# Kernel optimization log

Hardware: AMD Instinct MI355X
Metric: run time of the kernel (lower is better)

Reference implementation:

```python
import jax, jax.numpy as jnp
import numpy as np

B, L, D, V, K, H, HD, FFN = 64, 512, 256, 32000, 6, 4, 64, 512

def _ln(x, g, b):
    mu = x.mean(-1, keepdims=True)
    v = ((x - mu) ** 2).mean(-1, keepdims=True)
    return (x - mu) / jnp.sqrt(v + 1e-5) * g + b

def _pool(x, mask):
    # attention pooling: last real token attends over full sequence
    lengths = mask.sum(1)
    last = jnp.maximum(lengths - 1, 0)
    q = x[jnp.arange(x.shape[0]), last]                      # [B,D]
    scores = jnp.einsum('bd,bld->bl', q, x)
    scores = jnp.where(mask, scores, -60000.0)
    a = jax.nn.softmax(scores, axis=-1)
    return jnp.einsum('bl,bld->bd', a, x)

def _expert(x, mask, ln1g, ln1b, Wqkv, bqkv, Wo, bo, ln2g, ln2b, W1, b1, W2, b2):
    # pre-LN transformer block, eval mode (dropout = identity)
    Bx, Lx, _ = x.shape
    h = _ln(x, ln1g, ln1b)
    qkv = h @ Wqkv.T + bqkv                                   # [B,L,3D]
    q, k, v = jnp.split(qkv, 3, axis=-1)
    q = q.reshape(Bx, Lx, H, HD).transpose(0, 2, 1, 3)
    k = k.reshape(Bx, Lx, H, HD).transpose(0, 2, 1, 3)
    v = v.reshape(Bx, Lx, H, HD).transpose(0, 2, 1, 3)
    s = jnp.einsum('bhqd,bhkd->bhqk', q, k) / jnp.sqrt(jnp.float32(HD))
    s = jnp.where(mask[:, None, None, :], s, -1e9)            # key_padding_mask
    a = jax.nn.softmax(s, axis=-1)
    o = jnp.einsum('bhqk,bhkd->bhqd', a, v).transpose(0, 2, 1, 3).reshape(Bx, Lx, D)
    x = x + o @ Wo.T + bo
    h2 = _ln(x, ln2g, ln2b)
    ff = jax.nn.gelu(h2 @ W1.T + b1, approximate=False) @ W2.T + b2
    return x + ff

def _gru(z, m, Wih, Whh, bih, bhh):
    # torch.nn.GRUCell semantics
    gi = z @ Wih.T + bih
    gh = m @ Whh.T + bhh
    ir, iz, inn = jnp.split(gi, 3, axis=-1)
    hr, hz, hn = jnp.split(gh, 3, axis=-1)
    r = jax.nn.sigmoid(ir + hr)
    u = jax.nn.sigmoid(iz + hz)
    n = jnp.tanh(inn + r * hn)
    return (1.0 - u) * n + u * m

def setup_inputs():
    key = jax.random.key(0)
    ks = jax.random.split(key, 24)
    def nrm(k, shape, s=0.02):
        return jax.random.normal(k, shape, jnp.float32) * s
    lengths = jax.random.randint(ks[0], (B,), 1, L + 1)
    mask = jnp.arange(L)[None, :] < lengths[:, None]          # prefix mask, >=1 real token
    tokens = jnp.where(mask, jax.random.randint(ks[1], (B, L), 1, V), 0)
    return dict(
        tokens=tokens, mask=mask,
        tok_emb=nrm(ks[2], (V, D)).at[0].set(0.0),            # padding_idx=0
        pos_emb=nrm(ks[3], (L, D)),
        emb_ln_g=jnp.ones((D,)), emb_ln_b=jnp.zeros((D,)),
        ln1_g=jnp.ones((K, D)), ln1_b=jnp.zeros((K, D)),
        Wqkv=nrm(ks[4], (K, 3 * D, D)), bqkv=jnp.zeros((K, 3 * D)),
        Wo=nrm(ks[5], (K, D, D)), bo=jnp.zeros((K, D)),
        ln2_g=jnp.ones((K, D)), ln2_b=jnp.zeros((K, D)),
        W1=nrm(ks[6], (K, FFN, D)), b1=jnp.zeros((K, FFN)),
        W2=nrm(ks[7], (K, D, FFN)), b2=jnp.zeros((K, D)),
        gru_Wih=nrm(ks[8], (3 * D, D)), gru_Whh=nrm(ks[9], (3 * D, D)),
        gru_bih=jnp.zeros((3 * D,)), gru_bhh=jnp.zeros((3 * D,)),
        cls_W=nrm(ks[10], (V, D)), cls_b=jnp.zeros((V,)),
    )

def reference(tokens, mask, tok_emb, pos_emb, emb_ln_g, emb_ln_b, ln1_g, ln1_b, Wqkv, bqkv, Wo, bo, ln2_g, ln2_b, W1, b1, W2, b2, gru_Wih, gru_Whh, gru_bih, gru_bhh, cls_W, cls_b):
    x = _ln(tok_emb[tokens] + pos_emb[None, :tokens.shape[1]], emb_ln_g, emb_ln_b)
    m = jnp.zeros((tokens.shape[0], D), x.dtype)
    # sequential routing / phase-1: n_iter = K, chosen = t % K for all samples, no halting
    for t in range(K):
        e = t % K
        x = _expert(x, mask, ln1_g[e], ln1_b[e], Wqkv[e], bqkv[e], Wo[e], bo[e],
                    ln2_g[e], ln2_b[e], W1[e], b1[e], W2[e], b2[e])
        z = _pool(x, mask)
        m = _gru(z, m, gru_Wih, gru_Whh, gru_bih, gru_bhh)    # GRU memory update
    return _pool(x, mask) @ cls_W.T + cls_b                   # [B, V] logits
```

## Files before the change

### kernel.cpp

```cpp
#include <hip/hip_runtime.h>
#include <hip/hip_bf16.h>

#define BB 64
#define LL 512
#define DD 256
#define VV 32000
#define KK 6
#define HH 4
#define FF 512
#define MM (BB * LL)

typedef __hip_bfloat16 bf16;
typedef unsigned short ushort_t;
typedef __attribute__((ext_vector_type(8))) __bf16 bf16x8;
typedef __attribute__((ext_vector_type(4))) float f32x4;
#define MFMA __builtin_amdgcn_mfma_f32_16x16x32_bf16

__device__ __forceinline__ ushort_t f2bfbits(float x) {
  return __builtin_bit_cast(unsigned short, (__bf16)x);
}
__device__ __forceinline__ unsigned pkbf(float lo, float hi) {
  return (unsigned)f2bfbits(lo) | ((unsigned)f2bfbits(hi) << 16);
}
union U8 { unsigned u[4]; bf16x8 v; };

__device__ __forceinline__ void gl_lds16(const ushort_t* g, ushort_t* l) {
  __builtin_amdgcn_global_load_lds(
      (const __attribute__((address_space(1))) unsigned int*)g,
      (__attribute__((address_space(3))) unsigned int*)l, 16, 0, 0);
}

__device__ __forceinline__ float blk_sum(float v, float* red) {
  #pragma unroll
  for (int o = 32; o > 0; o >>= 1) v += __shfl_down(v, o, 64);
  __syncthreads();
  if ((threadIdx.x & 63) == 0) red[threadIdx.x >> 6] = v;
  __syncthreads();
  return red[0] + red[1] + red[2] + red[3];
}

__global__ __launch_bounds__(256) void k_lens(const int* __restrict__ tokens, int* __restrict__ lens) {
  __shared__ float red[4];
  int b = blockIdx.x, t = threadIdx.x;
  float c = (tokens[b * LL + t] != 0 ? 1.f : 0.f) + (tokens[b * LL + 256 + t] != 0 ? 1.f : 0.f);
  float s = blk_sum(c, red);
  if (t == 0) lens[b] = (int)(s + 0.5f);
}

__global__ __launch_bounds__(64) void k_order(const int* __restrict__ lens, int* __restrict__ order) {
  int b = threadIdx.x;
  __shared__ int L[64];
  int len = lens[b];
  L[b] = len;
  __syncthreads();
  int rank = 0;
  for (int i = 0; i < 64; i++) {
    int li = L[i];
    if (li > len || (li == len && i < b)) rank++;
  }
  order[rank] = b;
}

__global__ __launch_bounds__(256) void k_embed4(const int* __restrict__ tokens,
                                                const float* __restrict__ tok_emb,
                                                const float* __restrict__ pos_emb,
                                                const float* __restrict__ g,
                                                const float* __restrict__ be,
                                                const float* __restrict__ g1,
                                                const float* __restrict__ b1,
                                                float* __restrict__ X,
                                                bf16* __restrict__ H) {
  int wid = threadIdx.x >> 6, lane = threadIdx.x & 63;
  int row = blockIdx.x * 4 + wid;
  int l = row & (LL - 1);
  int tok = tokens[row];
  float4 a = *reinterpret_cast<const float4*>(tok_emb + (size_t)tok * DD + lane * 4);
  float4 p = *reinterpret_cast<const float4*>(pos_emb + (size_t)l * DD + lane * 4);
  float4 v = {a.x + p.x, a.y + p.y, a.z + p.z, a.w + p.w};
  float s = v.x + v.y + v.z + v.w;
  float q = v.x * v.x + v.y * v.y + v.z * v.z + v.w * v.w;
  #pragma unroll
  for (int o = 32; o > 0; o >>= 1) { s += __shfl_xor(s, o, 64); q += __shfl_xor(q, o, 64); }
  float mu = s * (1.f / DD);
  float rstd = rsqrtf(q * (1.f / DD) - mu * mu + 1e-5f);
  float4 gv = *reinterpret_cast<const float4*>(g + lane * 4);
  float4 bv = *reinterpret_cast<const float4*>(be + lane * 4);
  float4 o4 = {(v.x - mu) * rstd * gv.x + bv.x, (v.y - mu) * rstd * gv.y + bv.y,
               (v.z - mu) * rstd * gv.z + bv.z, (v.w - mu) * rstd * gv.w + bv.w};
  *reinterpret_cast<float4*>(X + (size_t)row * DD + lane * 4) = o4;
  float s2 = o4.x + o4.y + o4.z + o4.w;
  float q2 = o4.x * o4.x + o4.y * o4.y + o4.z * o4.z + o4.w * o4.w;
  #pragma unroll
  for (int o = 32; o > 0; o >>= 1) { s2 += __shfl_xor(s2, o, 64); q2 += __shfl_xor(q2, o, 64); }
  float mu2 = s2 * (1.f / DD);
  float rstd2 = rsqrtf(q2 * (1.f / DD) - mu2 * mu2 + 1e-5f);
  float4 g1v = *reinterpret_cast<const float4*>(g1 + lane * 4);
  float4 b1v = *reinterpret_cast<const float4*>(b1 + lane * 4);
  ushort4 h4;
  h4.x = f2bfbits((o4.x - mu2) * rstd2 * g1v.x + b1v.x);
  h4.y = f2bfbits((o4.y - mu2) * rstd2 * g1v.y + b1v.y);
  h4.z = f2bfbits((o4.z - mu2) * rstd2 * g1v.z + b1v.z);
  h4.w = f2bfbits((o4.w - mu2) * rstd2 * g1v.w + b1v.w);
  *reinterpret_cast<ushort4*>((ushort_t*)H + (size_t)row * DD + lane * 4) = h4;
}

__global__ __launch_bounds__(256) void k_cvtw(const float* __restrict__ w0, const float* __restrict__ w1,
                                              const float* __restrict__ w2, const float* __restrict__ w3,
                                              ushort_t* __restrict__ d) {
  int i = (blockIdx.x * 256 + threadIdx.x) * 4;
  const float* s; int off;
  if (i < 196608)      { s = w0; off = i; }
  else if (i < 262144) { s = w1; off = i - 196608; }
  else if (i < 393216) { s = w2; off = i - 262144; }
  else                 { s = w3; off = i - 393216; }
  float4 v = *reinterpret_cast<const float4*>(s + off);
  ushort4 o;
  o.x = f2bfbits(v.x); o.y = f2bfbits(v.y); o.z = f2bfbits(v.z); o.w = f2bfbits(v.w);
  *reinterpret_cast<ushort4*>(d + i) = o;
}

template <int MT, int NT, int KD, bool GELU, bool RES, bool OUTBF16, bool FUSELN>
__global__ __launch_bounds__(256) void k_mgemm(const ushort_t* __restrict__ A,
                                               const ushort_t* __restrict__ Wb,
                                               const float* __restrict__ bias,
                                               const float* __restrict__ res,
                                               void* __restrict__ outp,
                                               ushort_t* __restrict__ Hout,
                                               const float* __restrict__ lng,
                                               const float* __restrict__ lnb,
                                               const int* __restrict__ lens,
                                               int Ndim) {
  constexpr int JF = (MT == 128) ? (NT / 32) : (NT / 64);
  constexpr int AR = MT / 64, BR = NT / 64;
  constexpr int L = AR + BR;
  constexpr int NK = KD / 32;
  int n0 = blockIdx.x * NT, m0 = blockIdx.y * MT;
  if ((m0 & (LL - 1)) >= lens[m0 >> 9]) return;
  __shared__ __align__(16) ushort_t As[3][MT * 32];
  __shared__ __align__(16) ushort_t Bs[3][NT * 32];
  int t = threadIdx.x, lane = t & 63, w = t >> 6;
  int wr = (MT == 128) ? (w >> 1) * 64 : 0;
  int wc = (MT == 128) ? (w & 1) * (NT / 2) : w * (NT / 4);
  int fr = lane & 15, fg = lane >> 4;

  int ca = lane & 3;
  const ushort_t* gA[AR];
  #pragma unroll
  for (int ra = 0; ra < AR; ra++) {
    int row = ra * 64 + (t >> 2);
    gA[ra] = A + (size_t)(m0 + row) * KD + ((ca ^ ((row >> 1) & 3)) << 3);
  }
  const ushort_t* gB[BR];
  #pragma unroll
  for (int rb = 0; rb < BR; rb++) {
    int row = rb * 64 + (t >> 2);
    gB[rb] = Wb + (size_t)(n0 + row) * KD + ((ca ^ ((row >> 1) & 3)) << 3);
  }

  f32x4 acc[4][JF];
  #pragma unroll
  for (int i = 0; i < 4; i++)
    #pragma unroll
    for (int j = 0; j < JF; j++) acc[i][j] = (f32x4){0.f, 0.f, 0.f, 0.f};

  #define STAGE(bi, koff) { \
    _Pragma("unroll") for (int ra = 0; ra < AR; ra++) gl_lds16(gA[ra] + (koff), &As[bi][ra * 2048 + w * 512]); \
    _Pragma("unroll") for (int rb = 0; rb < BR; rb++) gl_lds16(gB[rb] + (koff), &Bs[bi][rb * 2048 + w * 512]); }

  STAGE(0, 0);
  #pragma unroll
  for (int kt = 0; kt < NK; kt++) {
    int cur = kt % 3;
    if (kt + 1 < NK) {
      STAGE((kt + 1) % 3, (kt + 1) * 32);
      asm volatile("s_waitcnt vmcnt(%0)" :: "n"(L) : "memory");
    } else {
      asm volatile("s_waitcnt vmcnt(0)" ::: "memory");
    }
    __builtin_amdgcn_s_barrier();
    __builtin_amdgcn_sched_barrier(0);
    bf16x8 af[4], bfr[JF];
    #pragma unroll
    for (int i = 0; i < 4; i++) {
      int row = wr + i * 16 + fr;
      af[i] = *reinterpret_cast<const bf16x8*>(&As[cur][row * 32 + ((fg ^ ((row >> 1) & 3)) << 3)]);
    }
    #pragma unroll
    for (int j = 0; j < JF; j++) {
      int row = wc + j * 16 + fr;
      bfr[j] = *reinterpret_cast<const bf16x8*>(&Bs[cur][row * 32 + ((fg ^ ((row >> 1) & 3)) << 3)]);
    }
    #pragma unroll
    for (int i = 0; i < 4; i++)
      #pragma unroll
      for (int j = 0; j < JF; j++)
        acc[i][j] = MFMA(af[i], bfr[j], acc[i][j], 0, 0, 0);
  }
  #undef STAGE

  if constexpr (!FUSELN) {
    #pragma unroll
    for (int i = 0; i < 4; i++) {
      int mbase = m0 + wr + i * 16 + fg * 4;
      #pragma unroll
      for (int j = 0; j < JF; j++) {
        int n = n0 + wc + j * 16 + fr;
        float bs = bias[n];
        #pragma unroll
        for (int r = 0; r < 4; r++) {
          int m = mbase + r;
          float v = acc[i][j][r] + bs;
          if (RES) v += res[(size_t)m * Ndim + n];
          if (GELU) v = 0.5f * v * (1.f + erff(v * 0.70710678118f));
          if (OUTBF16) ((ushort_t*)outp)[(size_t)m * Ndim + n] = f2bfbits(v);
          else         ((float*)outp)[(size_t)m * Ndim + n] = v;
        }
      }
    }
  } else {
    __shared__ float redS[4][64], redQ[4][64], lnmv[64], lnrv[64];
    float rs[4][4], rq[4][4];
    #pragma unroll
    for (int i = 0; i < 4; i++)
      #pragma unroll
      for (int r = 0; r < 4; r++) { rs[i][r] = 0.f; rq[i][r] = 0.f; }
    #pragma unroll
    for (int i = 0; i < 4; i++) {
      #pragma unroll
      for (int j = 0; j < 4; j++) {
        int n = wc + j * 16 + fr;
        float bs = bias[n];
        #pragma unroll
        for (int r = 0; r < 4; r++) {
          int m = m0 + i * 16 + fg * 4 + r;
          float v = acc[i][j][r] + bs;
          if (RES) v += res[(size_t)m * DD + n];
          acc[i][j][r] = v;
          ((float*)outp)[(size_t)m * DD + n] = v;
          rs[i][r] += v; rq[i][r] += v * v;
        }
      }
    }
    #pragma unroll
    for (int i = 0; i < 4; i++)
      #pragma unroll
      for (int r = 0; r < 4; r++) {
        float s = rs[i][r], q = rq[i][r];
        s += __shfl_xor(s, 1, 64); q += __shfl_xor(q, 1, 64);
        s += __shfl_xor(s, 2, 64); q += __shfl_xor(q, 2, 64);
        s += __shfl_xor(s, 4, 64); q += __shfl_xor(q, 4, 64);
        s += __shfl_xor(s, 8, 64); q += __shfl_xor(q, 8, 64);
        if (fr == 0) {
          redS[w][i * 16 + fg * 4 + r] = s;
          redQ[w][i * 16 + fg * 4 + r] = q;
        }
      }
    __syncthreads();
    if (t < 64) {
      float s = redS[0][t] + redS[1][t] + redS[2][t] + redS[3][t];
      float q = redQ[0][t] + redQ[1][t] + redQ[2][t] + redQ[3][t];
      float mu = s * (1.f / DD);
      lnmv[t] = mu;
      lnrv[t] = rsqrtf(q * (1.f / DD) - mu * mu + 1e-5f);
    }
    __syncthreads();
    #pragma unroll
    for (int i = 0; i < 4; i++) {
      #pragma unroll
      for (int j = 0; j < 4; j++) {
        int n = wc + j * 16 + fr;
        float gv = lng[n], bv = lnb[n];
        #pragma unroll
        for (int r = 0; r < 4; r++) {
          int rl = i * 16 + fg * 4 + r;
          float h = (acc[i][j][r] - lnmv[rl]) * lnrv[rl] * gv + bv;
          Hout[(size_t)(m0 + rl) * DD + n] = f2bfbits(h);
        }
      }
    }
  }
}

__global__ __launch_bounds__(512) void k_mattn7(const ushort_t* __restrict__ QKV,
                                                const int* __restrict__ lens,
                                                const int* __restrict__ order,
                                                ushort_t* __restrict__ O) {
  int b = order[blockIdx.z], h = blockIdx.y;
  int len = lens[b];
  int q0 = blockIdx.x * 128;
  if (q0 >= len) return;
  int t = threadIdx.x, lane = t & 63, w = t >> 6;
  int fr = lane & 15, fg = lane >> 4;
  __shared__ __align__(16) ushort_t Kh[8192];
  __shared__ __align__(16) ushort_t Vh[8192];

  const ushort_t* base = QKV + (size_t)b * LL * 768;
  int qw = q0 + w * 16;
  bool qact = qw < len;
  int q = qw + fr;

  const ushort_t* qp = base + (size_t)q * 768 + h * 64 + fg * 8;
  bf16x8 qf0 = *reinterpret_cast<const bf16x8*>(qp);
  bf16x8 qf1 = *reinterpret_cast<const bf16x8*>(qp + 32);

  const float SC = 0.125f * 1.44269504f;
  f32x4 ot[4];
  #pragma unroll
  for (int df = 0; df < 4; df++) ot[df] = (f32x4){0.f, 0.f, 0.f, 0.f};
  float m_run = -1e30f, lsum = 0.f;

  for (int kb = 0; kb < len; kb += 128) {
    if (kb) __syncthreads();
    int lim = min(128, len - kb);
    #pragma unroll
    for (int rr = 0; rr < 2; rr++) {
      if (rr * 64 >= lim) break;
      int krow = rr * 64 + w * 8 + (lane >> 3);
      int gk = kb + krow; if (gk > len - 1) gk = len - 1;
      int ch = lane & 7;
      const ushort_t* src = base + (size_t)gk * 768 + 256 + h * 64 + ((ch ^ (krow & 7)) << 3);
      gl_lds16(src, &Kh[rr * 4096 + w * 512]);
    }
    #pragma unroll
    for (int it = 0; it < 2; it++) {
      if (it * 64 >= lim) break;
      int c = it * 512 + t;
      int k = c >> 3, dg = c & 7;
      int gk = kb + k; if (gk > len - 1) gk = len - 1;
      uint4 vv = *reinterpret_cast<const uint4*>(base + (size_t)gk * 768 + 512 + h * 64 + dg * 8);
      unsigned uu[4] = {vv.x, vv.y, vv.z, vv.w};
      #pragma unroll
      for (int j = 0; j < 4; j++) {
        int d0 = dg * 8 + j * 2, d1 = d0 + 1;
        int s0 = (d0 ^ (d0 >> 3)) & 7, s1 = (d1 ^ (d1 >> 3)) & 7;
        Vh[d0 * 128 + (((k >> 3) ^ s0) << 3) + (k & 7)] = (ushort_t)(uu[j] & 0xffff);
        Vh[d1 * 128 + (((k >> 3) ^ s1) << 3) + (k & 7)] = (ushort_t)(uu[j] >> 16);
      }
    }
    __syncthreads();

    if (qact) {
      for (int kt = 0; kt < lim; kt += 64) {
        f32x4 s[4];
        __builtin_amdgcn_s_setprio(1);
        #pragma unroll
        for (int f = 0; f < 4; f++) {
          s[f] = (f32x4){0.f, 0.f, 0.f, 0.f};
          int krow = kt + f * 16 + fr;
          const ushort_t* kp0 = &Kh[krow * 64 + ((fg ^ (krow & 7)) << 3)];
          const ushort_t* kp1 = &Kh[krow * 64 + (((4 + fg) ^ (krow & 7)) << 3)];
          s[f] = MFMA(*reinterpret_cast<const bf16x8*>(kp0), qf0, s[f], 0, 0, 0);
          s[f] = MFMA(*reinterpret_cast<const bf16x8*>(kp1), qf1, s[f], 0, 0, 0);
        }
        __builtin_amdgcn_s_setprio(0);
        if (lim - kt >= 64) {
          #pragma unroll
          for (int f = 0; f < 4; f++)
            #pragma unroll
            for (int r = 0; r < 4; r++) s[f][r] *= SC;
        } else {
          int rem = lim - kt;
          #pragma unroll
          for (int f = 0; f < 4; f++)
            #pragma unroll
            for (int r = 0; r < 4; r++)
              s[f][r] = (f * 16 + fg * 4 + r < rem) ? s[f][r] * SC : -1e30f;
        }
        float tm = -1e30f;
        #pragma unroll
        for (int f = 0; f < 4; f++)
          #pragma unroll
          for (int r = 0; r < 4; r++) tm = fmaxf(tm, s[f][r]);
        tm = fmaxf(tm, __shfl_xor(tm, 16, 64));
        tm = fmaxf(tm, __shfl_xor(tm, 32, 64));
        bool grow = tm > m_run;
        if (__any(grow)) {
          float m_new = grow ? tm : m_run;
          float corr = exp2f(m_run - m_new);
          lsum *= corr;
          #pragma unroll
          for (int df = 0; df < 4; df++)
            #pragma unroll
            for (int r = 0; r < 4; r++) ot[df][r] *= corr;
          m_run = m_new;
        }
        float ps = 0.f;
        #pragma unroll
        for (int f = 0; f < 4; f++)
          #pragma unroll
          for (int r = 0; r < 4; r++) {
            float p = exp2f(s[f][r] - m_run);
            s[f][r] = p; ps += p;
          }
        ps += __shfl_xor(ps, 16, 64);
        ps += __shfl_xor(ps, 32, 64);
        lsum += ps;
        #pragma unroll
        for (int st = 0; st < 2; st++) {
          int fA = st * 2, fB = fA + 1;
          unsigned a0 = pkbf(s[fA][0], s[fA][1]), a1 = pkbf(s[fA][2], s[fA][3]);
          unsigned b0 = pkbf(s[fB][0], s[fB][1]), b1 = pkbf(s[fB][2], s[fB][3]);
          int sA = ((fg & 1) * 2) * 16 + fr;
          int sB = sA + 16;
          unsigned wa0 = __shfl(a0, sA, 64), wb0 = __shfl(b0, sA, 64);
          unsigned wa1 = __shfl(a1, sA, 64), wb1 = __shfl(b1, sA, 64);
          unsigned wa2 = __shfl(a0, sB, 64), wb2 = __shfl(b0, sB, 64);
          unsigned wa3 = __shfl(a1, sB, 64), wb3 = __shfl(b1, sB, 64);
          bool lo = fg < 2;
          U8 pf;
          pf.u[0] = lo ? wa0 : wb0; pf.u[1] = lo ? wa1 : wb1;
          pf.u[2] = lo ? wa2 : wb2; pf.u[3] = lo ? wa3 : wb3;
          int cb = (kt >> 3) + st * 4 + fg;
          __builtin_amdgcn_s_setprio(1);
          #pragma unroll
          for (int df = 0; df < 4; df++) {
            int d = df * 16 + fr;
            int sd = (d ^ (d >> 3)) & 7;
            const ushort_t* vp = &Vh[d * 128 + ((cb ^ sd) << 3)];
            ot[df] = MFMA(*reinterpret_cast<const bf16x8*>(vp), pf.v, ot[df], 0, 0, 0);
          }
          __builtin_amdgcn_s_setprio(0);
        }
      }
    }
  }

  if (q < len) {
    float linv = 1.f / lsum;
    #pragma unroll
    for (int df = 0; df < 4; df++) {
      ushort4 ov;
      ov.x = f2bfbits(ot[df][0] * linv);
      ov.y = f2bfbits(ot[df][1] * linv);
      ov.z = f2bfbits(ot[df][2] * linv);
      ov.w = f2bfbits(ot[df][3] * linv);
      *reinterpret_cast<ushort4*>(O + (size_t)(b * LL + q) * DD + h * 64 + df * 16 + fg * 4) = ov;
    }
  }
}

__global__ __launch_bounds__(256) void k_pool(const float* __restrict__ X,
                                              const int* __restrict__ lens,
                                              bf16* __restrict__ pooled) {
  __shared__ float red[4];
  __shared__ float qs[DD];
  __shared__ float sc[LL];
  int b = blockIdx.x, t = threadIdx.x;
  int len = lens[b];
  const float* Xb = X + (size_t)b * LL * DD;
  qs[t] = Xb[(size_t)(len - 1) * DD + t];
  __syncthreads();
  for (int l = t; l < LL; l += 256) {
    float s = -1e30f;
    if (l < len) {
      const float4* xr = reinterpret_cast<const float4*>(Xb + (size_t)l * DD);
      const float4* qq = reinterpret_cast<const float4*>(qs);
      float a0 = 0, a1 = 0, a2 = 0, a3 = 0;
      for (int k4 = 0; k4 < 64; k4++) {
        float4 xv = xr[k4], qv = qq[k4];
        a0 += xv.x * qv.x; a1 += xv.y * qv.y; a2 += xv.z * qv.z; a3 += xv.w * qv.w;
      }
      s = (a0 + a1) + (a2 + a3);
    }
    sc[l] = s;
  }
  __syncthreads();
  float mx = fmaxf(sc[t], sc[t + 256]);
  #pragma unroll
  for (int off = 32; off > 0; off >>= 1) mx = fmaxf(mx, __shfl_down(mx, off, 64));
  __syncthreads();
  if ((t & 63) == 0) red[t >> 6] = mx;
  __syncthreads();
  mx = fmaxf(fmaxf(red[0], red[1]), fmaxf(red[2], red[3]));
  float e0 = (t < len) ? __expf(sc[t] - mx) : 0.f;
  float e1 = (t + 256 < len) ? __expf(sc[t + 256] - mx) : 0.f;
  float ssum = blk_sum(e0 + e1, red);
  float inv = 1.f / ssum;
  __syncthreads();
  sc[t] = e0 * inv; sc[t + 256] = e1 * inv;
  __syncthreads();
  float acc = 0.f;
  for (int l = 0; l < len; l++) acc += sc[l] * Xb[(size_t)l * DD + t];
  pooled[b * DD + t] = __float2bfloat16(acc);
}

__global__ __launch_bounds__(512) void k_cls(const ushort_t* __restrict__ POOL,
                                             const float* __restrict__ W,
                                             const float* __restrict__ bias,
                                             float* __restrict__ out) {
  int t = threadIdx.x, lane = t & 63, w = t >> 6;
  int fr = lane & 15, fg = lane >> 4;
  int n = blockIdx.x * 128 + w * 16 + fr;
  const float* wp = W + (size_t)n * DD + fg * 8;
  f32x4 acc[4];
  #pragma unroll
  for (int i = 0; i < 4; i++) acc[i] = (f32x4){0.f, 0.f, 0.f, 0.f};
  for (int k0 = 0; k0 < DD; k0 += 32) {
    float4 f0 = *reinterpret_cast<const float4*>(wp + k0);
    float4 f1 = *reinterpret_cast<const float4*>(wp + k0 + 4);
    U8 bfr;
    bfr.u[0] = pkbf(f0.x, f0.y); bfr.u[1] = pkbf(f0.z, f0.w);
    bfr.u[2] = pkbf(f1.x, f1.y); bfr.u[3] = pkbf(f1.z, f1.w);
    #pragma unroll
    for (int i = 0; i < 4; i++) {
      bf16x8 af = *reinterpret_cast<const bf16x8*>(POOL + (size_t)(i * 16 + fr) * DD + k0 + fg * 8);
      acc[i] = MFMA(af, bfr.v, acc[i], 0, 0, 0);
    }
  }
  float bs = bias[n];
  #pragma unroll
  for (int i = 0; i < 4; i++)
    #pragma unroll
    for (int r = 0; r < 4; r++)
      out[(size_t)(i * 16 + fg * 4 + r) * VV + n] = acc[i][r] + bs;
}

extern "C" void kernel_launch(void* const* d_in, const int* in_sizes, int n_in,
                              void* d_out, int out_size, void* d_ws, size_t ws_size,
                              hipStream_t stream) {
  const int*   tokens  = (const int*)d_in[0];
  const float* tok_emb = (const float*)d_in[2];
  const float* pos_emb = (const float*)d_in[3];
  const float* emb_g   = (const float*)d_in[4];
  const float* emb_b   = (const float*)d_in[5];
  const float* ln1_g   = (const float*)d_in[6];
  const float* ln1_b   = (const float*)d_in[7];
  const float* Wqkv    = (const float*)d_in[8];
  const float* bqkv    = (const float*)d_in[9];
  const float* Wo      = (const float*)d_in[10];
  const float* bo      = (const float*)d_in[11];
  const float* ln2_g   = (const float*)d_in[12];
  const float* ln2_b   = (const float*)d_in[13];
  const float* W1      = (const float*)d_in[14];
  const float* b1      = (const float*)d_in[15];
  const float* W2      = (const float*)d_in[16];
  const float* b2      = (const float*)d_in[17];
  const float* cls_W   = (const float*)d_in[22];
  const float* cls_b   = (const float*)d_in[23];

  char* ws = (char*)d_ws;
  float*    X    = (float*)ws;
  ushort_t* QKV  = (ushort_t*)(ws + 33554432);
  ushort_t* Hb   = (ushort_t*)(ws + 83886080);
  ushort_t* WB   = (ushort_t*)(ws + 100663296);
  ushort_t* POOL = (ushort_t*)(ws + 101711872);
  int*      LEN  = (int*)(ws + 101744640);
  int*      ORD  = (int*)(ws + 101744896);

  const int OFF_QKV = 0, OFF_WO = 196608, OFF_W1 = 262144, OFF_W2 = 393216;

  k_lens<<<BB, 256, 0, stream>>>(tokens, LEN);
  k_order<<<1, 64, 0, stream>>>(LEN, ORD);
  k_embed4<<<MM / 4, 256, 0, stream>>>(tokens, tok_emb, pos_emb, emb_g, emb_b,
                                       ln1_g, ln1_b, X, (bf16*)Hb);

  for (int e = 0; e < KK; e++) {
    k_cvtw<<<512, 256, 0, stream>>>(Wqkv + (size_t)e * 196608, Wo + (size_t)e * 65536,
                                    W1 + (size_t)e * 131072, W2 + (size_t)e * 131072, WB);
    k_mgemm<128, 256, 256, false, false, true, false><<<dim3(3, 256), 256, 0, stream>>>(
        Hb, WB + OFF_QKV, bqkv + e * 3 * DD, nullptr, QKV, nullptr, nullptr, nullptr, LEN, 3 * DD);
    k_mattn7<<<dim3(4, HH, BB), 512, 0, stream>>>(QKV, LEN, ORD, Hb);
    k_mgemm<64, 256, 256, false, true, false, true><<<dim3(1, 512), 256, 0, stream>>>(
        Hb, WB + OFF_WO, bo + e * DD, X, X, Hb, ln2_g + e * DD, ln2_b + e * DD, LEN, DD);
    k_mgemm<128, 256, 256, true, false, true, false><<<dim3(2, 256), 256, 0, stream>>>(
        Hb, WB + OFF_W1, b1 + e * FF, nullptr, QKV, nullptr, nullptr, nullptr, LEN, FF);
    if (e < KK - 1) {
      k_mgemm<64, 256, 512, false, true, false, true><<<dim3(1, 512), 256, 0, stream>>>(
          QKV, WB + OFF_W2, b2 + e * DD, X, X, Hb,
          ln1_g + (e + 1) * DD, ln1_b + (e + 1) * DD, LEN, DD);
    } else {
      k_mgemm<64, 256, 512, false, true, false, false><<<dim3(1, 512), 256, 0, stream>>>(
          QKV, WB + OFF_W2, b2 + e * DD, X, X, nullptr, nullptr, nullptr, LEN, DD);
    }
  }

  k_pool<<<BB, 256, 0, stream>>>(X, LEN, (bf16*)POOL);
  k_cls<<<dim3(VV / 128), 512, 0, stream>>>(POOL, cls_W, cls_b, (float*)d_out);
}
```

Baseline: 808.8 us.

## Split attention keys across wave pairs and batch all weight conversions upfront

The attention kernel now covers 64 queries per block instead of 128. The two waves of each query strip take alternate 128-key halves of a 256-key chunk, and their partial softmax state is merged through LDS at the end (split-K flash attention). This doubles the grid and aims to fill the GPU better and cut per-block serial work, at the cost of twice the LDS and an extra merge step. Separately, the weight conversion to bf16 for all six experts is done in one launch before the loop, using a larger workspace, instead of one launch per expert.

Result: slower. 980.0 us (+21.2%).

```diff
diff --git a/kernel.cpp b/kernel.cpp
--- a/kernel.cpp
+++ b/kernel.cpp
@@ -104,16 +104,19 @@
   *reinterpret_cast<ushort4*>((ushort_t*)H + (size_t)row * DD + lane * 4) = h4;
 }
 
-__global__ __launch_bounds__(256) void k_cvtw(const float* __restrict__ w0, const float* __restrict__ w1,
-                                              const float* __restrict__ w2, const float* __restrict__ w3,
-                                              ushort_t* __restrict__ d) {
+__global__ __launch_bounds__(256) void k_cvtall(const float* __restrict__ Wqkv,
+                                                const float* __restrict__ Wo,
+                                                const float* __restrict__ W1,
+                                                const float* __restrict__ W2,
+                                                ushort_t* __restrict__ d) {
   int i = (blockIdx.x * 256 + threadIdx.x) * 4;
-  const float* s; int off;
-  if (i < 196608)      { s = w0; off = i; }
-  else if (i < 262144) { s = w1; off = i - 196608; }
-  else if (i < 393216) { s = w2; off = i - 262144; }
-  else                 { s = w3; off = i - 393216; }
-  float4 v = *reinterpret_cast<const float4*>(s + off);
+  int e = i / 524288, r = i - e * 524288;
+  const float* s;
+  if (r < 196608)      s = Wqkv + (size_t)e * 196608 + r;
+  else if (r < 262144) s = Wo + (size_t)e * 65536 + (r - 196608);
+  else if (r < 393216) s = W1 + (size_t)e * 131072 + (r - 262144);
+  else                 s = W2 + (size_t)e * 131072 + (r - 393216);
+  float4 v = *reinterpret_cast<const float4*>(s);
   ushort4 o;
   o.x = f2bfbits(v.x); o.y = f2bfbits(v.y); o.z = f2bfbits(v.z); o.w = f2bfbits(v.w);
   *reinterpret_cast<ushort4*>(d + i) = o;
@@ -281,21 +284,22 @@
   }
 }
 
-__global__ __launch_bounds__(512) void k_mattn7(const ushort_t* __restrict__ QKV,
+__global__ __launch_bounds__(512) void k_mattn8(const ushort_t* __restrict__ QKV,
                                                 const int* __restrict__ lens,
                                                 const int* __restrict__ order,
                                                 ushort_t* __restrict__ O) {
   int b = order[blockIdx.z], h = blockIdx.y;
   int len = lens[b];
-  int q0 = blockIdx.x * 128;
+  int q0 = blockIdx.x * 64;
   if (q0 >= len) return;
   int t = threadIdx.x, lane = t & 63, w = t >> 6;
+  int strip = w >> 1, ks = w & 1;
   int fr = lane & 15, fg = lane >> 4;
-  __shared__ __align__(16) ushort_t Kh[8192];
-  __shared__ __align__(16) ushort_t Vh[8192];
+  __shared__ __align__(16) ushort_t Kh[2][8192];
+  __shared__ __align__(16) ushort_t Vh[2][8192];
 
   const ushort_t* base = QKV + (size_t)b * LL * 768;
-  int qw = q0 + w * 16;
+  int qw = q0 + strip * 16;
   bool qact = qw < len;
   int q = qw + fr;
 
@@ -309,57 +313,61 @@
   for (int df = 0; df < 4; df++) ot[df] = (f32x4){0.f, 0.f, 0.f, 0.f};
   float m_run = -1e30f, lsum = 0.f;
 
-  for (int kb = 0; kb < len; kb += 128) {
-    if (kb) __syncthreads();
-    int lim = min(128, len - kb);
-    #pragma unroll
-    for (int rr = 0; rr < 2; rr++) {
-      if (rr * 64 >= lim) break;
-      int krow = rr * 64 + w * 8 + (lane >> 3);
-      int gk = kb + krow; if (gk > len - 1) gk = len - 1;
-      int ch = lane & 7;
-      const ushort_t* src = base + (size_t)gk * 768 + 256 + h * 64 + ((ch ^ (krow & 7)) << 3);
-      gl_lds16(src, &Kh[rr * 4096 + w * 512]);
-    }
-    #pragma unroll
-    for (int it = 0; it < 2; it++) {
-      if (it * 64 >= lim) break;
-      int c = it * 512 + t;
-      int k = c >> 3, dg = c & 7;
-      int gk = kb + k; if (gk > len - 1) gk = len - 1;
-      uint4 vv = *reinterpret_cast<const uint4*>(base + (size_t)gk * 768 + 512 + h * 64 + dg * 8);
-      unsigned uu[4] = {vv.x, vv.y, vv.z, vv.w};
-      #pragma unroll
-      for (int j = 0; j < 4; j++) {
-        int d0 = dg * 8 + j * 2, d1 = d0 + 1;
-        int s0 = (d0 ^ (d0 >> 3)) & 7, s1 = (d1 ^ (d1 >> 3)) & 7;
-        Vh[d0 * 128 + (((k >> 3) ^ s0) << 3) + (k & 7)] = (ushort_t)(uu[j] & 0xffff);
-        Vh[d1 * 128 + (((k >> 3) ^ s1) << 3) + (k & 7)] = (ushort_t)(uu[j] >> 16);
+  for (int kb2 = 0; kb2 < len; kb2 += 256) {
+    if (kb2) __syncthreads();
+    #pragma unroll
+    for (int ss = 0; ss < 2; ss++) {
+      int kbh = kb2 + ss * 128;
+      if (ss && kbh >= len) break;
+      #pragma unroll
+      for (int rr = 0; rr < 2; rr++) {
+        int krow = rr * 64 + w * 8 + (lane >> 3);
+        int gk = kbh + krow; if (gk > len - 1) gk = len - 1;
+        int ch = lane & 7;
+        const ushort_t* src = base + (size_t)gk * 768 + 256 + h * 64 + ((ch ^ (krow & 7)) << 3);
+        gl_lds16(src, &Kh[ss][rr * 4096 + w * 512]);
+      }
+      #pragma unroll
+      for (int it = 0; it < 2; it++) {
+        int c = it * 512 + t;
+        int k = c >> 3, dg = c & 7;
+        int gk = kbh + k; if (gk > len - 1) gk = len - 1;
+        uint4 vv = *reinterpret_cast<const uint4*>(base + (size_t)gk * 768 + 512 + h * 64 + dg * 8);
+        unsigned uu[4] = {vv.x, vv.y, vv.z, vv.w};
+        #pragma unroll
+        for (int j = 0; j < 4; j++) {
+          int d0 = dg * 8 + j * 2, d1 = d0 + 1;
+          int s0 = (d0 ^ (d0 >> 3)) & 7, s1 = (d1 ^ (d1 >> 3)) & 7;
+          Vh[ss][d0 * 128 + (((k >> 3) ^ s0) << 3) + (k & 7)] = (ushort_t)(uu[j] & 0xffff);
+          Vh[ss][d1 * 128 + (((k >> 3) ^ s1) << 3) + (k & 7)] = (ushort_t)(uu[j] >> 16);
+        }
       }
     }
     __syncthreads();
 
-    if (qact) {
-      for (int kt = 0; kt < lim; kt += 64) {
+    int kbw = kb2 + ks * 128;
+    int limw = min(128, len - kbw);
+    if (qact && limw > 0) {
+      for (int kt = 0; kt < limw; kt += 64) {
         f32x4 s[4];
         __builtin_amdgcn_s_setprio(1);
         #pragma unroll
         for (int f = 0; f < 4; f++) {
           s[f] = (f32x4){0.f, 0.f, 0.f, 0.f};
           int krow = kt + f * 16 + fr;
-          const ushort_t* kp0 = &Kh[krow * 64 + ((fg ^ (krow & 7)) << 3)];
-          const ushort_t* kp1 = &Kh[krow * 64 + (((4 + fg) ^ (krow & 7)) << 3)];
+          const ushort_t* kp0 = &Kh[ks][krow * 64 + ((fg ^ (krow & 7)) << 3)];
+          const ushort_t* kp1 = &Kh[ks][krow * 64 + (((4 + fg) ^ (krow & 7)) << 3)];
           s[f] = MFMA(*reinterpret_cast<const bf16x8*>(kp0), qf0, s[f], 0, 0, 0);
           s[f] = MFMA(*reinterpret_cast<const bf16x8*>(kp1), qf1, s[f], 0, 0, 0);
         }
         __builtin_amdgcn_s_setprio(0);
-        if (lim - kt >= 64) {
+        if (limw - kt >= 64) {
           #pragma unroll
           for (int f = 0; f < 4; f++)
             #pragma unroll
             for (int r = 0; r < 4; r++) s[f][r] *= SC;
         } else {
-          int rem = lim - kt;
+          int rem = limw - kt;
           #pragma unroll
           for (int f = 0; f < 4; f++)
             #pragma unroll
@@ -416,7 +424,7 @@
           for (int df = 0; df < 4; df++) {
             int d = df * 16 + fr;
             int sd = (d ^ (d >> 3)) & 7;
-            const ushort_t* vp = &Vh[d * 128 + ((cb ^ sd) << 3)];
+            const ushort_t* vp = &Vh[ks][d * 128 + ((cb ^ sd) << 3)];
             ot[df] = MFMA(*reinterpret_cast<const bf16x8*>(vp), pf.v, ot[df], 0, 0, 0);
           }
           __builtin_amdgcn_s_setprio(0);
@@ -425,15 +433,31 @@
     }
   }
 
-  if (q < len) {
-    float linv = 1.f / lsum;
+  __syncthreads();
+  float* MB = (float*)&Kh[0][0];
+  if (ks == 1) {
+    float* p = MB + ((size_t)(strip * 64 + lane)) * 18;
+    p[0] = m_run; p[1] = lsum;
+    #pragma unroll
+    for (int df = 0; df < 4; df++)
+      #pragma unroll
+      for (int r = 0; r < 4; r++) p[2 + df * 4 + r] = ot[df][r];
+  }
+  __syncthreads();
+  if (ks == 0 && q < len) {
+    const float* p = MB + ((size_t)(strip * 64 + lane)) * 18;
+    float m1 = p[0], l1 = p[1];
+    float m_new = fmaxf(m_run, m1);
+    float c0 = exp2f(m_run - m_new), c1 = exp2f(m1 - m_new);
+    float lt = lsum * c0 + l1 * c1;
+    float linv = 1.f / lt;
     #pragma unroll
     for (int df = 0; df < 4; df++) {
       ushort4 ov;
-      ov.x = f2bfbits(ot[df][0] * linv);
-      ov.y = f2bfbits(ot[df][1] * linv);
-      ov.z = f2bfbits(ot[df][2] * linv);
-      ov.w = f2bfbits(ot[df][3] * linv);
+      ov.x = f2bfbits((ot[df][0] * c0 + p[2 + df * 4 + 0] * c1) * linv);
+      ov.y = f2bfbits((ot[df][1] * c0 + p[2 + df * 4 + 1] * c1) * linv);
+      ov.z = f2bfbits((ot[df][2] * c0 + p[2 + df * 4 + 2] * c1) * linv);
+      ov.w = f2bfbits((ot[df][3] * c0 + p[2 + df * 4 + 3] * c1) * linv);
       *reinterpret_cast<ushort4*>(O + (size_t)(b * LL + q) * DD + h * 64 + df * 16 + fg * 4) = ov;
     }
   }
@@ -542,24 +566,25 @@
   float*    X    = (float*)ws;
   ushort_t* QKV  = (ushort_t*)(ws + 33554432);
   ushort_t* Hb   = (ushort_t*)(ws + 83886080);
-  ushort_t* WB   = (ushort_t*)(ws + 100663296);
-  ushort_t* POOL = (ushort_t*)(ws + 101711872);
-  int*      LEN  = (int*)(ws + 101744640);
-  int*      ORD  = (int*)(ws + 101744896);
+  ushort_t* WB6  = (ushort_t*)(ws + 100663296);
+  ushort_t* POOL = (ushort_t*)(ws + 106954752);
+  int*      LEN  = (int*)(ws + 106987520);
+  int*      ORD  = (int*)(ws + 106987776);
 
   const int OFF_QKV = 0, OFF_WO = 196608, OFF_W1 = 262144, OFF_W2 = 393216;
+  const int LW = 524288;
 
   k_lens<<<BB, 256, 0, stream>>>(tokens, LEN);
   k_order<<<1, 64, 0, stream>>>(LEN, ORD);
+  k_cvtall<<<3072, 256, 0, stream>>>(Wqkv, Wo, W1, W2, WB6);
   k_embed4<<<MM / 4, 256, 0, stream>>>(tokens, tok_emb, pos_emb, emb_g, emb_b,
                                        ln1_g, ln1_b, X, (bf16*)Hb);
 
   for (int e = 0; e < KK; e++) {
-    k_cvtw<<<512, 256, 0, stream>>>(Wqkv + (size_t)e * 196608, Wo + (size_t)e * 65536,
-                                    W1 + (size_t)e * 131072, W2 + (size_t)e * 131072, WB);
+    const ushort_t* WB = WB6 + (size_t)e * LW;
     k_mgemm<128, 256, 256, false, false, true, false><<<dim3(3, 256), 256, 0, stream>>>(
         Hb, WB + OFF_QKV, bqkv + e * 3 * DD, nullptr, QKV, nullptr, nullptr, nullptr, LEN, 3 * DD);
-    k_mattn7<<<dim3(4, HH, BB), 512, 0, stream>>>(QKV, LEN, ORD, Hb);
+    k_mattn8<<<dim3(8, HH, BB), 512, 0, stream>>>(QKV, LEN, ORD, Hb);
     k_mgemm<64, 256, 256, false, true, false, true><<<dim3(1, 512), 256, 0, stream>>>(
         Hb, WB + OFF_WO, bo + e * DD, X, X, Hb, ln2_g + e * DD, ln2_b + e * DD, LEN, DD);
     k_mgemm<128, 256, 256, true, false, true, false><<<dim3(2, 256), 256, 0, stream>>>(
```

## Write V transposed from QKV GEMM epilogue and batch weight conversion upfront

Applied to the files above, without the earlier changes.

The QKV GEMM epilogue now writes Q and K into a separate 512-wide buffer and stages V through shared memory, storing it transposed per (batch, head) as [d][L]. The attention kernel then loads V tiles with direct global-to-LDS copies instead of scalar transposing scatters into shared memory. Separately, all six experts' weights are converted to bf16 in one launch before the loop instead of one conversion per expert. The cost is an extra shared-memory round trip and barriers in the QKV epilogue, plus a larger workspace for the bf16 weights.

Result: no change. 798.3 us (-1.3%).

```diff
diff --git a/kernel.cpp b/kernel.cpp
--- a/kernel.cpp
+++ b/kernel.cpp
@@ -104,22 +104,25 @@
   *reinterpret_cast<ushort4*>((ushort_t*)H + (size_t)row * DD + lane * 4) = h4;
 }
 
-__global__ __launch_bounds__(256) void k_cvtw(const float* __restrict__ w0, const float* __restrict__ w1,
-                                              const float* __restrict__ w2, const float* __restrict__ w3,
-                                              ushort_t* __restrict__ d) {
+__global__ __launch_bounds__(256) void k_cvtall(const float* __restrict__ Wqkv,
+                                                const float* __restrict__ Wo,
+                                                const float* __restrict__ W1,
+                                                const float* __restrict__ W2,
+                                                ushort_t* __restrict__ d) {
   int i = (blockIdx.x * 256 + threadIdx.x) * 4;
-  const float* s; int off;
-  if (i < 196608)      { s = w0; off = i; }
-  else if (i < 262144) { s = w1; off = i - 196608; }
-  else if (i < 393216) { s = w2; off = i - 262144; }
-  else                 { s = w3; off = i - 393216; }
-  float4 v = *reinterpret_cast<const float4*>(s + off);
+  int e = i / 524288, r = i - e * 524288;
+  const float* s;
+  if (r < 196608)      s = Wqkv + (size_t)e * 196608 + r;
+  else if (r < 262144) s = Wo + (size_t)e * 65536 + (r - 196608);
+  else if (r < 393216) s = W1 + (size_t)e * 131072 + (r - 262144);
+  else                 s = W2 + (size_t)e * 131072 + (r - 393216);
+  float4 v = *reinterpret_cast<const float4*>(s);
   ushort4 o;
   o.x = f2bfbits(v.x); o.y = f2bfbits(v.y); o.z = f2bfbits(v.z); o.w = f2bfbits(v.w);
   *reinterpret_cast<ushort4*>(d + i) = o;
 }
 
-template <int MT, int NT, int KD, bool GELU, bool RES, bool OUTBF16, bool FUSELN>
+template <int MT, int NT, int KD, bool GELU, bool RES, bool OUTBF16, bool FUSELN, bool QKVT>
 __global__ __launch_bounds__(256) void k_mgemm(const ushort_t* __restrict__ A,
                                                const ushort_t* __restrict__ Wb,
                                                const float* __restrict__ bias,
@@ -134,10 +137,12 @@
   constexpr int AR = MT / 64, BR = NT / 64;
   constexpr int L = AR + BR;
   constexpr int NK = KD / 32;
+  constexpr int ASZ = 3 * MT * 32;
   int n0 = blockIdx.x * NT, m0 = blockIdx.y * MT;
   if ((m0 & (LL - 1)) >= lens[m0 >> 9]) return;
-  __shared__ __align__(16) ushort_t As[3][MT * 32];
-  __shared__ __align__(16) ushort_t Bs[3][NT * 32];
+  __shared__ __align__(16) ushort_t SH[ASZ + 3 * NT * 32];
+  ushort_t* As = SH;
+  ushort_t* Bs = SH + ASZ;
   int t = threadIdx.x, lane = t & 63, w = t >> 6;
   int wr = (MT == 128) ? (w >> 1) * 64 : 0;
   int wc = (MT == 128) ? (w & 1) * (NT / 2) : w * (NT / 4);
@@ -164,8 +169,8 @@
     for (int j = 0; j < JF; j++) acc[i][j] = (f32x4){0.f, 0.f, 0.f, 0.f};
 
   #define STAGE(bi, koff) { \
-    _Pragma("unroll") for (int ra = 0; ra < AR; ra++) gl_lds16(gA[ra] + (koff), &As[bi][ra * 2048 + w * 512]); \
-    _Pragma("unroll") for (int rb = 0; rb < BR; rb++) gl_lds16(gB[rb] + (koff), &Bs[bi][rb * 2048 + w * 512]); }
+    _Pragma("unroll") for (int ra = 0; ra < AR; ra++) gl_lds16(gA[ra] + (koff), &As[(bi) * MT * 32 + ra * 2048 + w * 512]); \
+    _Pragma("unroll") for (int rb = 0; rb < BR; rb++) gl_lds16(gB[rb] + (koff), &Bs[(bi) * NT * 32 + rb * 2048 + w * 512]); }
 
   STAGE(0, 0);
   #pragma unroll
@@ -183,12 +188,12 @@
     #pragma unroll
     for (int i = 0; i < 4; i++) {
       int row = wr + i * 16 + fr;
-      af[i] = *reinterpret_cast<const bf16x8*>(&As[cur][row * 32 + ((fg ^ ((row >> 1) & 3)) << 3)]);
+      af[i] = *reinterpret_cast<const bf16x8*>(&As[cur * MT * 32 + row * 32 + ((fg ^ ((row >> 1) & 3)) << 3)]);
     }
     #pragma unroll
     for (int j = 0; j < JF; j++) {
       int row = wc + j * 16 + fr;
-      bfr[j] = *reinterpret_cast<const bf16x8*>(&Bs[cur][row * 32 + ((fg ^ ((row >> 1) & 3)) << 3)]);
+      bfr[j] = *reinterpret_cast<const bf16x8*>(&Bs[cur * NT * 32 + row * 32 + ((fg ^ ((row >> 1) & 3)) << 3)]);
     }
     #pragma unroll
     for (int i = 0; i < 4; i++)
@@ -198,7 +203,45 @@
   }
   #undef STAGE
 
-  if constexpr (!FUSELN) {
+  if constexpr (QKVT) {
+    if (n0 < 512) {
+      #pragma unroll
+      for (int i = 0; i < 4; i++) {
+        int mbase = m0 + wr + i * 16 + fg * 4;
+        #pragma unroll
+        for (int j = 0; j < JF; j++) {
+          int n = n0 + wc + j * 16 + fr;
+          float bs = bias[n];
+          #pragma unroll
+          for (int r = 0; r < 4; r++)
+            ((ushort_t*)outp)[(size_t)(mbase + r) * 512 + n] = f2bfbits(acc[i][j][r] + bs);
+        }
+      }
+    } else {
+      __syncthreads();
+      #pragma unroll
+      for (int i = 0; i < 4; i++) {
+        #pragma unroll
+        for (int j = 0; j < JF; j++) {
+          int dfull = wc + j * 16 + fr;
+          float bs = bias[512 + dfull];
+          int kl = wr + i * 16 + fg * 4;
+          #pragma unroll
+          for (int r = 0; r < 4; r++)
+            SH[dfull * 136 + kl + r] = f2bfbits(acc[i][j][r] + bs);
+        }
+      }
+      __syncthreads();
+      int bidx = m0 >> 9, k0 = m0 & (LL - 1);
+      #pragma unroll
+      for (int it = 0; it < 16; it++) {
+        int g = it * 256 + t;
+        int row = g >> 4, mc = g & 15;
+        uint4 val = *reinterpret_cast<const uint4*>(&SH[row * 136 + mc * 8]);
+        *reinterpret_cast<uint4*>(Hout + (((size_t)(bidx * 4 + (row >> 6)) * 64 + (row & 63)) << 9) + k0 + mc * 8) = val;
+      }
+    }
+  } else if constexpr (!FUSELN) {
     #pragma unroll
     for (int i = 0; i < 4; i++) {
       int mbase = m0 + wr + i * 16 + fg * 4;
@@ -281,7 +324,8 @@
   }
 }
 
-__global__ __launch_bounds__(512) void k_mattn7(const ushort_t* __restrict__ QKV,
+__global__ __launch_bounds__(512) void k_mattn9(const ushort_t* __restrict__ QK,
+                                                const ushort_t* __restrict__ VT,
                                                 const int* __restrict__ lens,
                                                 const int* __restrict__ order,
                                                 ushort_t* __restrict__ O) {
@@ -294,14 +338,14 @@
   __shared__ __align__(16) ushort_t Kh[8192];
   __shared__ __align__(16) ushort_t Vh[8192];
 
-  const ushort_t* base = QKV + (size_t)b * LL * 768;
   int qw = q0 + w * 16;
   bool qact = qw < len;
   int q = qw + fr;
 
-  const ushort_t* qp = base + (size_t)q * 768 + h * 64 + fg * 8;
+  const ushort_t* qp = QK + (size_t)(b * LL + q) * 512 + h * 64 + fg * 8;
   bf16x8 qf0 = *reinterpret_cast<const bf16x8*>(qp);
   bf16x8 qf1 = *reinterpret_cast<const bf16x8*>(qp + 32);
+  const ushort_t* vbase = VT + (((size_t)(b * 4 + h) * 64) << 9);
 
   const float SC = 0.125f * 1.44269504f;
   f32x4 ot[4];
@@ -318,24 +362,17 @@
       int krow = rr * 64 + w * 8 + (lane >> 3);
       int gk = kb + krow; if (gk > len - 1) gk = len - 1;
       int ch = lane & 7;
-      const ushort_t* src = base + (size_t)gk * 768 + 256 + h * 64 + ((ch ^ (krow & 7)) << 3);
+      const ushort_t* src = QK + (size_t)(b * LL + gk) * 512 + 256 + h * 64 + ((ch ^ (krow & 7)) << 3);
       gl_lds16(src, &Kh[rr * 4096 + w * 512]);
     }
     #pragma unroll
-    for (int it = 0; it < 2; it++) {
-      if (it * 64 >= lim) break;
-      int c = it * 512 + t;
-      int k = c >> 3, dg = c & 7;
-      int gk = kb + k; if (gk > len - 1) gk = len - 1;
-      uint4 vv = *reinterpret_cast<const uint4*>(base + (size_t)gk * 768 + 512 + h * 64 + dg * 8);
-      unsigned uu[4] = {vv.x, vv.y, vv.z, vv.w};
-      #pragma unroll
-      for (int j = 0; j < 4; j++) {
-        int d0 = dg * 8 + j * 2, d1 = d0 + 1;
-        int s0 = (d0 ^ (d0 >> 3)) & 7, s1 = (d1 ^ (d1 >> 3)) & 7;
-        Vh[d0 * 128 + (((k >> 3) ^ s0) << 3) + (k & 7)] = (ushort_t)(uu[j] & 0xffff);
-        Vh[d1 * 128 + (((k >> 3) ^ s1) << 3) + (k & 7)] = (ushort_t)(uu[j] >> 16);
-      }
+    for (int rr = 0; rr < 2; rr++) {
+      int d = rr * 32 + w * 4 + (lane >> 4);
+      int ch = lane & 15;
+      int sd = (d ^ (d >> 3)) & 7;
+      int chs = (ch & 8) | ((ch & 7) ^ sd);
+      const ushort_t* src = vbase + ((size_t)d << 9) + kb + (chs << 3);
+      gl_lds16(src, &Vh[rr * 4096 + w * 512]);
     }
     __syncthreads();
 
@@ -540,37 +577,39 @@
 
   char* ws = (char*)d_ws;
   float*    X    = (float*)ws;
-  ushort_t* QKV  = (ushort_t*)(ws + 33554432);
+  ushort_t* QKb  = (ushort_t*)(ws + 33554432);
+  ushort_t* VTg  = (ushort_t*)(ws + 67108864);
   ushort_t* Hb   = (ushort_t*)(ws + 83886080);
-  ushort_t* WB   = (ushort_t*)(ws + 100663296);
-  ushort_t* POOL = (ushort_t*)(ws + 101711872);
-  int*      LEN  = (int*)(ws + 101744640);
-  int*      ORD  = (int*)(ws + 101744896);
+  ushort_t* WB6  = (ushort_t*)(ws + 100663296);
+  ushort_t* POOL = (ushort_t*)(ws + 106954752);
+  int*      LEN  = (int*)(ws + 106987520);
+  int*      ORD  = (int*)(ws + 106987776);
 
   const int OFF_QKV = 0, OFF_WO = 196608, OFF_W1 = 262144, OFF_W2 = 393216;
+  const int LW = 524288;
 
   k_lens<<<BB, 256, 0, stream>>>(tokens, LEN);
   k_order<<<1, 64, 0, stream>>>(LEN, ORD);
+  k_cvtall<<<3072, 256, 0, stream>>>(Wqkv, Wo, W1, W2, WB6);
   k_embed4<<<MM / 4, 256, 0, stream>>>(tokens, tok_emb, pos_emb, emb_g, emb_b,
                                        ln1_g, ln1_b, X, (bf16*)Hb);
 
   for (int e = 0; e < KK; e++) {
-    k_cvtw<<<512, 256, 0, stream>>>(Wqkv + (size_t)e * 196608, Wo + (size_t)e * 65536,
-                                    W1 + (size_t)e * 131072, W2 + (size_t)e * 131072, WB);
-    k_mgemm<128, 256, 256, false, false, true, false><<<dim3(3, 256), 256, 0, stream>>>(
-        Hb, WB + OFF_QKV, bqkv + e * 3 * DD, nullptr, QKV, nullptr, nullptr, nullptr, LEN, 3 * DD);
-    k_mattn7<<<dim3(4, HH, BB), 512, 0, stream>>>(QKV, LEN, ORD, Hb);
-    k_mgemm<64, 256, 256, false, true, false, true><<<dim3(1, 512), 256, 0, stream>>>(
+    const ushort_t* WB = WB6 + (size_t)e * LW;
+    k_mgemm<128, 256, 256, false, false, true, false, true><<<dim3(3, 256), 256, 0, stream>>>(
+        Hb, WB + OFF_QKV, bqkv + e * 3 * DD, nullptr, QKb, VTg, nullptr, nullptr, LEN, 3 * DD);
+    k_mattn9<<<dim3(4, HH, BB), 512, 0, stream>>>(QKb, VTg, LEN, ORD, Hb);
+    k_mgemm<64, 256, 256, false, true, false, true, false><<<dim3(1, 512), 256, 0, stream>>>(
         Hb, WB + OFF_WO, bo + e * DD, X, X, Hb, ln2_g + e * DD, ln2_b + e * DD, LEN, DD);
-    k_mgemm<128, 256, 256, true, false, true, false><<<dim3(2, 256), 256, 0, stream>>>(
-        Hb, WB + OFF_W1, b1 + e * FF, nullptr, QKV, nullptr, nullptr, nullptr, LEN, FF);
+    k_mgemm<128, 256, 256, true, false, true, false, false><<<dim3(2, 256), 256, 0, stream>>>(
+        Hb, WB + OFF_W1, b1 + e * FF, nullptr, QKb, nullptr, nullptr, nullptr, LEN, FF);
     if (e < KK - 1) {
-      k_mgemm<64, 256, 512, false, true, false, true><<<dim3(1, 512), 256, 0, stream>>>(
-          QKV, WB + OFF_W2, b2 + e * DD, X, X, Hb,
+      k_mgemm<64, 256, 512, false, true, false, true, false><<<dim3(1, 512), 256, 0, stream>>>(
+          QKb, WB + OFF_W2, b2 + e * DD, X, X, Hb,
           ln1_g + (e + 1) * DD, ln1_b + (e + 1) * DD, LEN, DD);
     } else {
-      k_mgemm<64, 256, 512, false, true, false, false><<<dim3(1, 512), 256, 0, stream>>>(
-          QKV, WB + OFF_W2, b2 + e * DD, X, X, nullptr, nullptr, nullptr, LEN, DD);
+      k_mgemm<64, 256, 512, false, true, false, false, false><<<dim3(1, 512), 256, 0, stream>>>(
+          QKb, WB + OFF_W2, b2 + e * DD, X, X, nullptr, nullptr, nullptr, LEN, DD);
     }
   }
 
```
